# Kernel tuning notes

Hardware: AMD Instinct MI355X
Metric: run time of the kernel (lower is better)

The kernel has to match this reference:

```python
import jax, jax.numpy as jnp
import numpy as np

N = 10000
E = 160000
IN_DIM = 256
PROJ_DIM = 512
HIDDEN = 512
OUT_DIM = 512
HEADS1, HEADS2, HEADS3 = 4, 4, 1
NEG_SLOPE = 0.2  # PyG GATConv default


def gat_conv(x, edge_index, W, att_src, att_dst, bias, heads, out_c, concat):
    """PyG GATConv (eval mode), with self-loops already appended to edge_index.
    x: [N, F_in]; W: [F_in, heads*out_c]; att_src/att_dst: [heads, out_c]; bias: [heads*out_c] or [out_c]."""
    n = x.shape[0]
    h = (x @ W).reshape(n, heads, out_c)            # [N, H, C]
    a_src = jnp.einsum('nhc,hc->nh', h, att_src)     # [N, H]
    a_dst = jnp.einsum('nhc,hc->nh', h, att_dst)     # [N, H]
    src, dst = edge_index[0], edge_index[1]
    e = jax.nn.leaky_relu(a_src[src] + a_dst[dst], NEG_SLOPE)  # [E, H]
    # segment softmax over incoming edges per destination node
    e_max = jax.ops.segment_max(e, dst, num_segments=n)
    e_exp = jnp.exp(e - e_max[dst])
    denom = jax.ops.segment_sum(e_exp, dst, num_segments=n)
    alpha = e_exp / denom[dst]                       # [E, H]
    msg = alpha[:, :, None] * h[src]                 # [E, H, C]
    out = jax.ops.segment_sum(msg, dst, num_segments=n)  # [N, H, C]
    out = out.reshape(n, heads * out_c) if concat else out.mean(axis=1)
    return out + bias


def setup_inputs() -> dict:
    key = jax.random.key(0)
    ks = jax.random.split(key, 16)
    g = 0.1
    inp = {
        'x': jax.random.normal(ks[0], (N, IN_DIM), dtype=jnp.float32),
        'edge_index': jax.random.randint(ks[1], (2, E), 0, N, dtype=jnp.int64),
        'proj_W': jax.random.normal(ks[2], (IN_DIM, PROJ_DIM), dtype=jnp.float32) * g,
        'proj_b': jnp.zeros((PROJ_DIM,), dtype=jnp.float32),
        'W1': jax.random.normal(ks[3], (PROJ_DIM, HEADS1 * HIDDEN), dtype=jnp.float32) * g,
        'as1': jax.random.normal(ks[4], (HEADS1, HIDDEN), dtype=jnp.float32) * g,
        'ad1': jax.random.normal(ks[5], (HEADS1, HIDDEN), dtype=jnp.float32) * g,
        'b1': jnp.zeros((HEADS1 * HIDDEN,), dtype=jnp.float32),
        'W2': jax.random.normal(ks[6], (HEADS1 * HIDDEN, HEADS2 * HIDDEN), dtype=jnp.float32) * g * 0.5,
        'as2': jax.random.normal(ks[7], (HEADS2, HIDDEN), dtype=jnp.float32) * g,
        'ad2': jax.random.normal(ks[8], (HEADS2, HIDDEN), dtype=jnp.float32) * g,
        'b2': jnp.zeros((HEADS2 * HIDDEN,), dtype=jnp.float32),
        'W3': jax.random.normal(ks[9], (HEADS2 * HIDDEN, HEADS3 * OUT_DIM), dtype=jnp.float32) * g * 0.5,
        'as3': jax.random.normal(ks[10], (HEADS3, OUT_DIM), dtype=jnp.float32) * g,
        'ad3': jax.random.normal(ks[11], (HEADS3, OUT_DIM), dtype=jnp.float32) * g,
        'b3': jnp.zeros((OUT_DIM,), dtype=jnp.float32),
    }
    return inp


def reference(x, edge_index, proj_W, proj_b, W1, as1, ad1, b1, W2, as2, ad2, b2, W3, as3, ad3, b3):
    # append self-loops once (PyG GATConv add_self_loops=True)
    loops = jnp.arange(N, dtype=edge_index.dtype)
    ei = jnp.concatenate([edge_index, jnp.stack([loops, loops])], axis=1)
    h = x @ proj_W + proj_b                                   # [N, 512]
    h = jax.nn.elu(gat_conv(h, ei, W1, as1, ad1, b1, HEADS1, HIDDEN, True))
    h = jax.nn.elu(gat_conv(h, ei, W2, as2, ad2, b2, HEADS2, HIDDEN, True))
    return gat_conv(h, ei, W3, as3, ad3, b3, HEADS3, OUT_DIM, False)  # [N, 512]
```

## Files before the change

kernel.cpp:

```cpp
#include <hip/hip_runtime.h>
#include <hip/hip_bf16.h>


#define LB(x) __launch_bounds__(x)

typedef unsigned short u16;
typedef unsigned int u32;
typedef __attribute__((ext_vector_type(8))) short short8;
typedef __attribute__((ext_vector_type(8))) short bf16x8;
typedef __attribute__((ext_vector_type(8))) _Float16 f16x8;
typedef __attribute__((ext_vector_type(4))) float f32x4;

__device__ __forceinline__ float b2f(u16 u) {
    union { float f; u32 u; } x;
    x.u = ((u32)u) << 16;
    return x.f;
}
__device__ __forceinline__ u16 f2b(float f) {
    u32 u = __float_as_uint(f);
    u = (u + 0x7FFFu + ((u >> 16) & 1u)) >> 16;
    return (u16)u;
}
__device__ __forceinline__ u16 f2h(float f) {
    union { _Float16 h; u16 u; } x;
    x.h = (_Float16)f;
    return x.u;
}
__device__ __forceinline__ float h2f(u16 u) {
    union { _Float16 h; u16 u; } x;
    x.u = u;
    return (float)x.h;
}
__device__ __forceinline__ void lds_cp16(const void* g, void* l) {
    __builtin_amdgcn_global_load_lds(
        (const __attribute__((address_space(1))) unsigned int*)g,
        (__attribute__((address_space(3))) unsigned int*)l, 16, 0, 0);
}

__global__ void k_deg(const int* __restrict__ ei, int E, int Np, int* __restrict__ deg) {
    int e = blockIdx.x * blockDim.x + threadIdx.x;
    if (e >= E + Np) return;
    int dst = (e < E) ? ei[E + e] : (e - E);
    atomicAdd(&deg[dst], 1);
}

__global__ LB(256) void k_s1(const int* __restrict__ deg, int* __restrict__ row_ptr,
                             int* __restrict__ bsum, int n) {
    __shared__ int sh[256];
    int b = blockIdx.x, t = threadIdx.x;
    int i = b * 256 + t;
    int v = (i < n) ? deg[i] : 0;
    sh[t] = v;
    __syncthreads();
    #pragma unroll
    for (int off = 1; off < 256; off <<= 1) {
        int add = (t >= off) ? sh[t - off] : 0;
        __syncthreads();
        sh[t] += add;
        __syncthreads();
    }
    if (i < n) row_ptr[i + 1] = sh[t];
    if (t == 255) bsum[b] = sh[255];
}

__global__ LB(64) void k_s2(int* __restrict__ bsum, int* __restrict__ boff, int nb) {
    __shared__ int sh[64];
    int t = threadIdx.x;
    sh[t] = (t < nb) ? bsum[t] : 0;
    __syncthreads();
    #pragma unroll
    for (int off = 1; off < 64; off <<= 1) {
        int add = (t >= off) ? sh[t - off] : 0;
        __syncthreads();
        sh[t] += add;
        __syncthreads();
    }
    if (t < nb) boff[t] = (t == 0) ? 0 : sh[t - 1];
}

__global__ LB(256) void k_s3(const int* __restrict__ deg, int* __restrict__ row_ptr,
                             const int* __restrict__ boff, int* __restrict__ cursor, int n) {
    int b = blockIdx.x, t = threadIdx.x;
    int i = b * 256 + t;
    if (i == 0) row_ptr[0] = 0;
    if (i < n) {
        int inc = row_ptr[i + 1] + boff[b];
        row_ptr[i + 1] = inc;
        cursor[i] = inc - deg[i];
    }
}

__global__ void k_fill(const int* __restrict__ ei, int E, int Np,
                       int* __restrict__ cursor, int* __restrict__ col_src) {
    int e = blockIdx.x * blockDim.x + threadIdx.x;
    if (e >= E + Np) return;
    int src, dst;
    if (e < E) { src = ei[e]; dst = ei[E + e]; }
    else       { src = dst = e - E; }
    int pos = atomicAdd(&cursor[dst], 1);
    col_src[pos] = src;
}

__global__ void k_pack(const float* __restrict__ in, u16* __restrict__ hi,
                       u16* __restrict__ lo, int n4) {
    int i = blockIdx.x * blockDim.x + threadIdx.x;
    if (i >= n4) return;
    float4 v = ((const float4*)in)[i];
    ushort4 h, l;
    h.x = f2b(v.x); l.x = f2b(v.x - b2f(h.x));
    h.y = f2b(v.y); l.y = f2b(v.y - b2f(h.y));
    h.z = f2b(v.z); l.z = f2b(v.z - b2f(h.z));
    h.w = f2b(v.w); l.w = f2b(v.w - b2f(h.w));
    ((ushort4*)hi)[i] = h;
    ((ushort4*)lo)[i] = l;
}

template<bool F16S>
__global__ LB(256) void k_wt_pack(const float* __restrict__ W, u16* __restrict__ Whi,
                                  u16* __restrict__ Wlo, int K, int Nn) {
    __shared__ float sh[32][33];
    int n0 = blockIdx.x * 32, k0 = blockIdx.y * 32;
    int c = threadIdx.x & 31, r0 = threadIdx.x >> 5;
    #pragma unroll
    for (int r = r0; r < 32; r += 8)
        sh[r][c] = W[(size_t)(k0 + r) * Nn + n0 + c];
    __syncthreads();
    #pragma unroll
    for (int r = r0; r < 32; r += 8) {
        float v = sh[c][r];
        if (F16S) {
            Whi[(size_t)(n0 + r) * K + k0 + c] = f2h(v);
        } else {
            u16 hi = f2b(v);
            Whi[(size_t)(n0 + r) * K + k0 + c] = hi;
            Wlo[(size_t)(n0 + r) * K + k0 + c] = f2b(v - b2f(hi));
        }
    }
}

__global__ LB(64) void k_bfold(const float* __restrict__ pb,
                               const u16* __restrict__ w1t_hi, const u16* __restrict__ w1t_lo,
                               float* __restrict__ bfold, int K) {
    int n = blockIdx.x;
    int lane = threadIdx.x;
    float s = 0.f;
    for (int k = lane; k < K; k += 64) {
        float w = b2f(w1t_hi[(size_t)n * K + k]) + b2f(w1t_lo[(size_t)n * K + k]);
        s = fmaf(pb[k], w, s);
    }
    #pragma unroll
    for (int off = 32; off; off >>= 1) s += __shfl_xor(s, off);
    if (lane == 0) bfold[n] = s;
}

template<int WM, int NFR, int PREC, int OUTMODE, bool ATT>
__global__ __launch_bounds__(WM * 128)
void k_gemm_pl(const u16* __restrict__ Ahi, const u16* __restrict__ Alo,
               const u16* __restrict__ Bhi, const u16* __restrict__ Blo,
               const float* __restrict__ bias,
               u16* __restrict__ Chi, u16* __restrict__ Clo,
               u16* __restrict__ Cf16,
               const float* __restrict__ att_s, const float* __restrict__ att_d,
               float* __restrict__ a_src, float* __restrict__ a_dst,
               int HH, int M, int K, int Nn) {
    constexpr int BM = WM * 64;
    constexpr int BN = NFR * 32;
    constexpr int T  = WM * 128;
    constexpr int BITER = (NFR * 128) / T > 0 ? (NFR * 128) / T : 1;
    constexpr int ALO_SZ = (PREC == 0) ? BM * 32 : 8;
    constexpr int BLO_SZ = (PREC == 0) ? BN * 32 : 8;
    __shared__ u16 AsHi[BM * 32];
    __shared__ u16 AsLo[ALO_SZ];
    __shared__ u16 BsHi[BN * 32];
    __shared__ u16 BsLo[BLO_SZ];
    const int tid  = threadIdx.x;
    const int lane = tid & 63;
    const int w    = tid >> 6;
    const int wr   = w >> 1;
    const int wc   = w & 1;
    const int row0 = blockIdx.y * BM;
    const int col0 = blockIdx.x * BN;
    const int ln15 = lane & 15;
    const int lq   = lane >> 4;

    f32x4 acc[4][NFR];
    #pragma unroll
    for (int m = 0; m < 4; ++m)
        #pragma unroll
        for (int n = 0; n < NFR; ++n) acc[m][n] = (f32x4){0.f, 0.f, 0.f, 0.f};

    for (int k0 = 0; k0 < K; k0 += 32) {
        #pragma unroll
        for (int i = 0; i < 2; ++i) {
            int c = i * T + tid;
            int r  = 2 * (c >> 3) + (((c >> 2) ^ (c >> 4)) & 1);
            int kc = (c & 3) ^ (r & 3);
            int gra = row0 + r; if (gra >= M) gra = M - 1;
            size_t ga = (size_t)gra * K + k0 + kc * 8;
            lds_cp16(Ahi + ga, (char*)AsHi + c * 16);
            if (PREC == 0) lds_cp16(Alo + ga, (char*)AsLo + c * 16);
        }
        #pragma unroll
        for (int i = 0; i < BITER; ++i) {
            int c = i * T + tid;
            int r  = 2 * (c >> 3) + (((c >> 2) ^ (c >> 4)) & 1);
            int kc = (c & 3) ^ (r & 3);
            size_t gb = (size_t)(col0 + r) * K + k0 + kc * 8;
            lds_cp16(Bhi + gb, (char*)BsHi + c * 16);
            if (PREC == 0) lds_cp16(Blo + gb, (char*)BsLo + c * 16);
        }
        __syncthreads();
        if (PREC == 0) {
            bf16x8 ah[4], al[4], bh[NFR], bl[NFR];
            #pragma unroll
            for (int m = 0; m < 4; ++m) {
                int row = wr * 64 + m * 16 + ln15;
                int byo = (row * 64 + lq * 16) ^ ((row & 7) << 4);
                ah[m] = *(const bf16x8*)((const char*)AsHi + byo);
                al[m] = *(const bf16x8*)((const char*)AsLo + byo);
            }
            #pragma unroll
            for (int n = 0; n < NFR; ++n) {
                int row = wc * (NFR * 16) + n * 16 + ln15;
                int byo = (row * 64 + lq * 16) ^ ((row & 7) << 4);
                bh[n] = *(const bf16x8*)((const char*)BsHi + byo);
                bl[n] = *(const bf16x8*)((const char*)BsLo + byo);
            }
            #pragma unroll
            for (int m = 0; m < 4; ++m)
                #pragma unroll
                for (int n = 0; n < NFR; ++n) {
                    acc[m][n] = __builtin_amdgcn_mfma_f32_16x16x32_bf16(al[m], bh[n], acc[m][n], 0, 0, 0);
                    acc[m][n] = __builtin_amdgcn_mfma_f32_16x16x32_bf16(ah[m], bl[n], acc[m][n], 0, 0, 0);
                    acc[m][n] = __builtin_amdgcn_mfma_f32_16x16x32_bf16(ah[m], bh[n], acc[m][n], 0, 0, 0);
                }
        } else {
            f16x8 a[4], b[NFR];
            #pragma unroll
            for (int m = 0; m < 4; ++m) {
                int row = wr * 64 + m * 16 + ln15;
                int byo = (row * 64 + lq * 16) ^ ((row & 7) << 4);
                a[m] = *(const f16x8*)((const char*)AsHi + byo);
            }
            #pragma unroll
            for (int n = 0; n < NFR; ++n) {
                int row = wc * (NFR * 16) + n * 16 + ln15;
                int byo = (row * 64 + lq * 16) ^ ((row & 7) << 4);
                b[n] = *(const f16x8*)((const char*)BsHi + byo);
            }
            #pragma unroll
            for (int m = 0; m < 4; ++m)
                #pragma unroll
                for (int n = 0; n < NFR; ++n)
                    acc[m][n] = __builtin_amdgcn_mfma_f32_16x16x32_f16(a[m], b[n], acc[m][n], 0, 0, 0);
        }
        __syncthreads();
    }

    #pragma unroll
    for (int m = 0; m < 4; ++m) {
        #pragma unroll
        for (int n = 0; n < NFR; ++n) {
            int gc = col0 + wc * (NFR * 16) + n * 16 + ln15;
            float badd = bias ? bias[gc] : 0.f;
            #pragma unroll
            for (int j = 0; j < 4; ++j) {
                int gr = row0 + wr * 64 + m * 16 + lq * 4 + j;
                if (gr < M) {
                    float v = acc[m][n][j] + badd;
                    size_t o = (size_t)gr * Nn + gc;
                    if (OUTMODE == 0) {
                        u16 hi = f2b(v);
                        Chi[o] = hi;
                        Clo[o] = f2b(v - b2f(hi));
                    } else {
                        Cf16[o] = f2h(v);
                    }
                }
            }
        }
    }

    if (ATT) {
        float atts[NFR], attd[NFR], bb[NFR];
        #pragma unroll
        for (int n = 0; n < NFR; ++n) {
            int gc = col0 + wc * (NFR * 16) + n * 16 + ln15;
            atts[n] = att_s[gc];
            attd[n] = att_d[gc];
            bb[n]   = bias ? bias[gc] : 0.f;
        }
        const int head = (col0 + wc * (NFR * 16)) >> 9;
        #pragma unroll
        for (int m = 0; m < 4; ++m) {
            #pragma unroll
            for (int j = 0; j < 4; ++j) {
                int gr = row0 + wr * 64 + m * 16 + lq * 4 + j;
                float s1 = 0.f, s2 = 0.f;
                #pragma unroll
                for (int n = 0; n < NFR; ++n) {
                    float v = acc[m][n][j] + bb[n];
                    s1 = fmaf(v, atts[n], s1);
                    s2 = fmaf(v, attd[n], s2);
                }
                #pragma unroll
                for (int off = 1; off < 16; off <<= 1) {
                    s1 += __shfl_xor(s1, off);
                    s2 += __shfl_xor(s2, off);
                }
                if (ln15 == 0 && gr < M) {
                    atomicAdd(&a_src[gr * HH + head], s1);
                    atomicAdd(&a_dst[gr * HH + head], s2);
                }
            }
        }
    }
}

template <int HH, int OMODE, bool ELU_>
__global__ __launch_bounds__(HH * 64)
void k_sagg(const int* __restrict__ row_ptr, const int* __restrict__ col_src,
            const float* __restrict__ a_src, const float* __restrict__ a_dst,
            const u16* __restrict__ hf, const float* __restrict__ bias,
            u16* __restrict__ Oh, float* __restrict__ Of, int C) {
    __shared__ float sal[HH * 64];
    const int d    = blockIdx.x;
    const int tid  = threadIdx.x;
    const int w    = tid >> 6;
    const int lane = tid & 63;
    const int F    = HH * C;
    const int o    = tid * 8;
    const int s = row_ptr[d], eend = row_ptr[d + 1];
    const int cnt = eend - s;
    const float adh = a_dst[d * HH + w];

    float acc[8];
    #pragma unroll
    for (int j = 0; j < 8; ++j) acc[j] = 0.f;

    if (cnt <= 64) {
        bool act = lane < cnt;
        float av = act ? a_src[col_src[s + lane] * HH + w] : 0.f;
        float x = av + adh;
        x = (x > 0.f) ? x : 0.2f * x;
        float v = act ? x : -1e30f;
        float m = v;
        #pragma unroll
        for (int off = 32; off; off >>= 1) m = fmaxf(m, __shfl_xor(m, off));
        float e_ = act ? __expf(v - m) : 0.f;
        float sum = e_;
        #pragma unroll
        for (int off = 32; off; off >>= 1) sum += __shfl_xor(sum, off);
        if (act) sal[w * 64 + lane] = e_ / sum;
        __syncthreads();

        if (cnt > 0) {
            short8 vv; float a;
            {
                int src0 = col_src[s];
                a = sal[w * 64];
                vv = *(const short8*)(hf + (size_t)src0 * F + o);
            }
            for (int i = 0; i < cnt; ++i) {
                short8 w_; float an;
                bool more = (i + 1 < cnt);
                if (more) {
                    int srcn = col_src[s + i + 1];
                    an = sal[w * 64 + i + 1];
                    w_ = *(const short8*)(hf + (size_t)srcn * F + o);
                }
                #pragma unroll
                for (int j = 0; j < 8; ++j)
                    acc[j] = fmaf(a, h2f((u16)vv[j]), acc[j]);
                if (more) { a = an; vv = w_; }
            }
        }
    } else {
        float m = -1e30f;
        for (int e = s + lane; e < eend; e += 64) {
            float x = a_src[col_src[e] * HH + w] + adh;
            x = (x > 0.f) ? x : 0.2f * x;
            m = fmaxf(m, x);
        }
        #pragma unroll
        for (int off = 32; off; off >>= 1) m = fmaxf(m, __shfl_xor(m, off));
        float sum = 0.f;
        for (int e = s + lane; e < eend; e += 64) {
            float x = a_src[col_src[e] * HH + w] + adh;
            x = (x > 0.f) ? x : 0.2f * x;
            sum += __expf(x - m);
        }
        #pragma unroll
        for (int off = 32; off; off >>= 1) sum += __shfl_xor(sum, off);
        float inv = 1.0f / sum;
        for (int base = s; base < eend; base += 64) {
            int e = base + lane;
            if (e < eend) {
                float x = a_src[col_src[e] * HH + w] + adh;
                x = (x > 0.f) ? x : 0.2f * x;
                sal[w * 64 + lane] = __expf(x - m) * inv;
            }
            __syncthreads();
            int nn = (eend - base < 64) ? (eend - base) : 64;
            for (int i = 0; i < nn; ++i) {
                int src = col_src[base + i];
                float a = sal[w * 64 + i];
                short8 vv = *(const short8*)(hf + (size_t)src * F + o);
                #pragma unroll
                for (int j = 0; j < 8; ++j)
                    acc[j] = fmaf(a, h2f((u16)vv[j]), acc[j]);
            }
            __syncthreads();
        }
    }

    #pragma unroll
    for (int j = 0; j < 8; ++j) {
        acc[j] += bias[o + j];
        if (ELU_) acc[j] = (acc[j] > 0.f) ? acc[j] : __expf(acc[j]) - 1.f;
    }
    if (OMODE == 0) {
        short8 r;
        #pragma unroll
        for (int j = 0; j < 8; ++j) r[j] = (short)f2h(acc[j]);
        *(short8*)(Oh + (size_t)d * F + o) = r;
    } else {
        float* po = Of + (size_t)d * F + o;
        #pragma unroll
        for (int j4 = 0; j4 < 2; ++j4) {
            float4 r;
            r.x = acc[j4 * 4 + 0]; r.y = acc[j4 * 4 + 1];
            r.z = acc[j4 * 4 + 2]; r.w = acc[j4 * 4 + 3];
            *(float4*)&po[j4 * 4] = r;
        }
    }
}

extern "C" void kernel_launch(void* const* d_in, const int* in_sizes, int n_in,
                              void* d_out, int out_size, void* d_ws, size_t ws_size,
                              hipStream_t stream) {
    const float* x      = (const float*)d_in[0];
    const int*   ei     = (const int*)d_in[1];
    const float* proj_W = (const float*)d_in[2];
    const float* proj_b = (const float*)d_in[3];
    const float* W1  = (const float*)d_in[4];
    const float* as1 = (const float*)d_in[5];
    const float* ad1 = (const float*)d_in[6];
    const float* b1  = (const float*)d_in[7];
    const float* W2  = (const float*)d_in[8];
    const float* as2 = (const float*)d_in[9];
    const float* ad2 = (const float*)d_in[10];
    const float* b2  = (const float*)d_in[11];
    const float* W3  = (const float*)d_in[12];
    const float* as3 = (const float*)d_in[13];
    const float* ad3 = (const float*)d_in[14];
    const float* b3  = (const float*)d_in[15];

    const int N  = in_sizes[0] / 256;
    const int E  = in_sizes[1] / 2;
    const int Ep = E + N;
    const int NB = (N + 255) / 256;

    size_t off = 0;
    auto alloc = [&](size_t bytes) -> void* {
        void* p = (char*)d_ws + off;
        off += (bytes + 255) & ~(size_t)255;
        return p;
    };
    u16* bufX    = (u16*)alloc((size_t)N * 2048 * 2);
    u16* bufY    = (u16*)alloc((size_t)N * 2048 * 2);
    u16* xb_hi   = (u16*)alloc((size_t)N * 256 * 2);
    u16* xb_lo   = (u16*)alloc((size_t)N * 256 * 2);
    u16* pw_hi   = (u16*)alloc((size_t)256 * 512 * 2);
    u16* pw_lo   = (u16*)alloc((size_t)256 * 512 * 2);
    u16* wf_hi   = (u16*)alloc((size_t)2048 * 256 * 2);
    u16* wf_lo   = (u16*)alloc((size_t)2048 * 256 * 2);
    float* bfold   = (float*)alloc((size_t)2048 * 4);
    float* att_z   = (float*)alloc((size_t)N * 18 * 4);
    int*   deg     = (int*)alloc((size_t)N * 4);
    int*   cursor  = (int*)alloc((size_t)N * 4);
    int*   row_ptr = (int*)alloc((size_t)(N + 1) * 4);
    int*   col_src = (int*)alloc((size_t)Ep * 4);
    int*   bsum    = (int*)alloc((size_t)NB * 4);
    int*   boff    = (int*)alloc((size_t)NB * 4);
    (void)ws_size;

    float* a_src1 = att_z;
    float* a_dst1 = att_z + (size_t)N * 4;
    float* a_src2 = att_z + (size_t)N * 8;
    float* a_dst2 = att_z + (size_t)N * 12;
    float* a_src3 = att_z + (size_t)N * 16;
    float* a_dst3 = att_z + (size_t)N * 17;

    u16* whi = (u16*)d_out;
    u16* wlo = (u16*)d_out + (size_t)2048 * 2048;

    hipMemsetAsync(deg, 0, (size_t)N * 4, stream);
    hipMemsetAsync(att_z, 0, (size_t)N * 18 * 4, stream);
    int eb = (Ep + 255) / 256;
    k_deg<<<eb, 256, 0, stream>>>(ei, E, N, deg);
    k_s1<<<NB, 256, 0, stream>>>(deg, row_ptr, bsum, N);
    k_s2<<<1, 64, 0, stream>>>(bsum, boff, NB);
    k_s3<<<NB, 256, 0, stream>>>(deg, row_ptr, boff, cursor, N);
    k_fill<<<eb, 256, 0, stream>>>(ei, E, N, cursor, col_src);

    const int MB1 = (N + 127) / 128;
    const int MB2 = (N + 255) / 256;

    k_pack<<<(N * 256 / 4 + 255) / 256, 256, 0, stream>>>(x, xb_hi, xb_lo, N * 256 / 4);
    k_pack<<<(256 * 512 / 4 + 255) / 256, 256, 0, stream>>>(proj_W, pw_hi, pw_lo, 256 * 512 / 4);

    k_wt_pack<false><<<dim3(2048 / 32, 512 / 32), 256, 0, stream>>>(W1, whi, wlo, 512, 2048);
    k_bfold<<<2048, 64, 0, stream>>>(proj_b, whi, wlo, bfold, 512);
    k_gemm_pl<2, 2, 0, 0, false><<<dim3(256 / 64, 2048 / 128), 256, 0, stream>>>(
        whi, wlo, pw_hi, pw_lo, nullptr, wf_hi, wf_lo, nullptr,
        nullptr, nullptr, nullptr, nullptr, 0, 2048, 512, 256);

    k_gemm_pl<2, 4, 0, 2, true><<<dim3(2048 / 128, MB1), 256, 0, stream>>>(
        xb_hi, xb_lo, wf_hi, wf_lo, bfold, nullptr, nullptr, bufX,
        as1, ad1, a_src1, a_dst1, 4, N, 256, 2048);
    k_sagg<4, 0, true><<<N, 256, 0, stream>>>(row_ptr, col_src, a_src1, a_dst1,
                                              bufX, b1, bufY, nullptr, 512);

    k_wt_pack<true><<<dim3(2048 / 32, 2048 / 32), 256, 0, stream>>>(W2, whi, nullptr, 2048, 2048);
    k_gemm_pl<4, 4, 2, 2, true><<<dim3(2048 / 128, MB2), 512, 0, stream>>>(
        bufY, nullptr, whi, nullptr, nullptr, nullptr, nullptr, bufX,
        as2, ad2, a_src2, a_dst2, 4, N, 2048, 2048);
    k_sagg<4, 0, true><<<N, 256, 0, stream>>>(row_ptr, col_src, a_src2, a_dst2,
                                              bufX, b2, bufY, nullptr, 512);

    k_wt_pack<true><<<dim3(512 / 32, 2048 / 32), 256, 0, stream>>>(W3, whi, nullptr, 2048, 512);
    k_gemm_pl<2, 2, 2, 2, true><<<dim3(512 / 64, MB1), 256, 0, stream>>>(
        bufY, nullptr, whi, nullptr, nullptr, nullptr, nullptr, bufX,
        as3, ad3, a_src3, a_dst3, 1, N, 2048, 512);
    k_sagg<1, 1, false><<<N, 64, 0, stream>>>(row_ptr, col_src, a_src3, a_dst3,
                                              bufX, b3, nullptr, (float*)d_out, 512);
}
```

Baseline: 623.8 us.

## Double-buffer LDS tiles in layer 2/3 GEMMs and unroll aggregation gather by two

Adds a double-buffered LDS mode to the GEMM kernel. The next K-tile's async copies are issued into the alternate buffer while the current tile is computed, which removes one barrier per iteration and hides global-load latency. It is enabled for the two f16 GEMMs with K=2048. Separately, the small-degree aggregation loop now keeps two neighbour rows in flight instead of one, to increase memory-level parallelism. The cost is doubled shared memory in those GEMMs, which may lower occupancy, and more registers in the gather loop.

```diff
diff --git a/kernel.cpp b/kernel.cpp
--- a/kernel.cpp
+++ b/kernel.cpp
@@ -153,7 +153,7 @@
     if (lane == 0) bfold[n] = s;
 }
 
-template<int WM, int NFR, int PREC, int OUTMODE, bool ATT>
+template<int WM, int NFR, int PREC, int OUTMODE, bool ATT, bool DB>
 __global__ __launch_bounds__(WM * 128)
 void k_gemm_pl(const u16* __restrict__ Ahi, const u16* __restrict__ Alo,
                const u16* __restrict__ Bhi, const u16* __restrict__ Blo,
@@ -166,13 +166,14 @@
     constexpr int BM = WM * 64;
     constexpr int BN = NFR * 32;
     constexpr int T  = WM * 128;
-    constexpr int BITER = (NFR * 128) / T > 0 ? (NFR * 128) / T : 1;
-    constexpr int ALO_SZ = (PREC == 0) ? BM * 32 : 8;
-    constexpr int BLO_SZ = (PREC == 0) ? BN * 32 : 8;
-    __shared__ u16 AsHi[BM * 32];
-    __shared__ u16 AsLo[ALO_SZ];
-    __shared__ u16 BsHi[BN * 32];
-    __shared__ u16 BsLo[BLO_SZ];
+    constexpr int BITER = ((NFR * 128) / T > 0) ? (NFR * 128) / T : 1;
+    constexpr int NBUF = DB ? 2 : 1;
+    constexpr int ASZ = BM * 32;
+    constexpr int BSZ = BN * 32;
+    __shared__ u16 AsHi[NBUF * ASZ];
+    __shared__ u16 AsLo[(PREC == 0) ? NBUF * ASZ : 8];
+    __shared__ u16 BsHi[NBUF * BSZ];
+    __shared__ u16 BsLo[(PREC == 0) ? NBUF * BSZ : 8];
     const int tid  = threadIdx.x;
     const int lane = tid & 63;
     const int w    = tid >> 6;
@@ -189,7 +190,9 @@
         #pragma unroll
         for (int n = 0; n < NFR; ++n) acc[m][n] = (f32x4){0.f, 0.f, 0.f, 0.f};
 
-    for (int k0 = 0; k0 < K; k0 += 32) {
+    auto STAGE = [&](int k0, int buf) {
+        size_t ab = (size_t)buf * ASZ * 2;
+        size_t bb = (size_t)buf * BSZ * 2;
         #pragma unroll
         for (int i = 0; i < 2; ++i) {
             int c = i * T + tid;
@@ -197,8 +200,8 @@
             int kc = (c & 3) ^ (r & 3);
             int gra = row0 + r; if (gra >= M) gra = M - 1;
             size_t ga = (size_t)gra * K + k0 + kc * 8;
-            lds_cp16(Ahi + ga, (char*)AsHi + c * 16);
-            if (PREC == 0) lds_cp16(Alo + ga, (char*)AsLo + c * 16);
+            lds_cp16(Ahi + ga, (char*)AsHi + ab + c * 16);
+            if (PREC == 0) lds_cp16(Alo + ga, (char*)AsLo + ab + c * 16);
         }
         #pragma unroll
         for (int i = 0; i < BITER; ++i) {
@@ -206,25 +209,29 @@
             int r  = 2 * (c >> 3) + (((c >> 2) ^ (c >> 4)) & 1);
             int kc = (c & 3) ^ (r & 3);
             size_t gb = (size_t)(col0 + r) * K + k0 + kc * 8;
-            lds_cp16(Bhi + gb, (char*)BsHi + c * 16);
-            if (PREC == 0) lds_cp16(Blo + gb, (char*)BsLo + c * 16);
-        }
-        __syncthreads();
+            lds_cp16(Bhi + gb, (char*)BsHi + bb + c * 16);
+            if (PREC == 0) lds_cp16(Blo + gb, (char*)BsLo + bb + c * 16);
+        }
+    };
+
+    auto COMPUTE = [&](int buf) {
+        size_t ab = (size_t)buf * ASZ * 2;
+        size_t bb = (size_t)buf * BSZ * 2;
         if (PREC == 0) {
             bf16x8 ah[4], al[4], bh[NFR], bl[NFR];
             #pragma unroll
             for (int m = 0; m < 4; ++m) {
                 int row = wr * 64 + m * 16 + ln15;
-                int byo = (row * 64 + lq * 16) ^ ((row & 7) << 4);
-                ah[m] = *(const bf16x8*)((const char*)AsHi + byo);
-                al[m] = *(const bf16x8*)((const char*)AsLo + byo);
+                size_t byo = (size_t)((row * 64 + lq * 16) ^ ((row & 7) << 4));
+                ah[m] = *(const bf16x8*)((const char*)AsHi + ab + byo);
+                al[m] = *(const bf16x8*)((const char*)AsLo + ab + byo);
             }
             #pragma unroll
             for (int n = 0; n < NFR; ++n) {
                 int row = wc * (NFR * 16) + n * 16 + ln15;
-                int byo = (row * 64 + lq * 16) ^ ((row & 7) << 4);
-                bh[n] = *(const bf16x8*)((const char*)BsHi + byo);
-                bl[n] = *(const bf16x8*)((const char*)BsLo + byo);
+                size_t byo = (size_t)((row * 64 + lq * 16) ^ ((row & 7) << 4));
+                bh[n] = *(const bf16x8*)((const char*)BsHi + bb + byo);
+                bl[n] = *(const bf16x8*)((const char*)BsLo + bb + byo);
             }
             #pragma unroll
             for (int m = 0; m < 4; ++m)
@@ -239,14 +246,14 @@
             #pragma unroll
             for (int m = 0; m < 4; ++m) {
                 int row = wr * 64 + m * 16 + ln15;
-                int byo = (row * 64 + lq * 16) ^ ((row & 7) << 4);
-                a[m] = *(const f16x8*)((const char*)AsHi + byo);
+                size_t byo = (size_t)((row * 64 + lq * 16) ^ ((row & 7) << 4));
+                a[m] = *(const f16x8*)((const char*)AsHi + ab + byo);
             }
             #pragma unroll
             for (int n = 0; n < NFR; ++n) {
                 int row = wc * (NFR * 16) + n * 16 + ln15;
-                int byo = (row * 64 + lq * 16) ^ ((row & 7) << 4);
-                b[n] = *(const f16x8*)((const char*)BsHi + byo);
+                size_t byo = (size_t)((row * 64 + lq * 16) ^ ((row & 7) << 4));
+                b[n] = *(const f16x8*)((const char*)BsHi + bb + byo);
             }
             #pragma unroll
             for (int m = 0; m < 4; ++m)
@@ -254,7 +261,25 @@
                 for (int n = 0; n < NFR; ++n)
                     acc[m][n] = __builtin_amdgcn_mfma_f32_16x16x32_f16(a[m], b[n], acc[m][n], 0, 0, 0);
         }
+    };
+
+    if (DB) {
+        const int nt = K >> 5;
+        STAGE(0, 0);
         __syncthreads();
+        for (int t = 0; t < nt; ++t) {
+            int cur = t & 1;
+            if (t + 1 < nt) STAGE((t + 1) << 5, cur ^ 1);
+            COMPUTE(cur);
+            __syncthreads();
+        }
+    } else {
+        for (int k0 = 0; k0 < K; k0 += 32) {
+            STAGE(k0, 0);
+            __syncthreads();
+            COMPUTE(0);
+            __syncthreads();
+        }
     }
 
     #pragma unroll
@@ -354,26 +379,25 @@
         if (act) sal[w * 64 + lane] = e_ / sum;
         __syncthreads();
 
-        if (cnt > 0) {
-            short8 vv; float a;
-            {
-                int src0 = col_src[s];
-                a = sal[w * 64];
-                vv = *(const short8*)(hf + (size_t)src0 * F + o);
-            }
-            for (int i = 0; i < cnt; ++i) {
-                short8 w_; float an;
-                bool more = (i + 1 < cnt);
-                if (more) {
-                    int srcn = col_src[s + i + 1];
-                    an = sal[w * 64 + i + 1];
-                    w_ = *(const short8*)(hf + (size_t)srcn * F + o);
-                }
-                #pragma unroll
-                for (int j = 0; j < 8; ++j)
-                    acc[j] = fmaf(a, h2f((u16)vv[j]), acc[j]);
-                if (more) { a = an; vv = w_; }
-            }
+        short8 v0, v1; float a0, a1;
+        if (cnt > 0) { v0 = *(const short8*)(hf + (size_t)col_src[s] * F + o); a0 = sal[w * 64]; }
+        if (cnt > 1) { v1 = *(const short8*)(hf + (size_t)col_src[s + 1] * F + o); a1 = sal[w * 64 + 1]; }
+        int i = 0;
+        for (; i + 2 <= cnt; i += 2) {
+            short8 t0, t1; float b0, b1;
+            bool m0 = (i + 2 < cnt), m1 = (i + 3 < cnt);
+            if (m0) { t0 = *(const short8*)(hf + (size_t)col_src[s + i + 2] * F + o); b0 = sal[w * 64 + i + 2]; }
+            if (m1) { t1 = *(const short8*)(hf + (size_t)col_src[s + i + 3] * F + o); b1 = sal[w * 64 + i + 3]; }
+            #pragma unroll
+            for (int j = 0; j < 8; ++j) acc[j] = fmaf(a0, h2f((u16)v0[j]), acc[j]);
+            #pragma unroll
+            for (int j = 0; j < 8; ++j) acc[j] = fmaf(a1, h2f((u16)v1[j]), acc[j]);
+            if (m0) { v0 = t0; a0 = b0; }
+            if (m1) { v1 = t1; a1 = b1; }
+        }
+        if (i < cnt) {
+            #pragma unroll
+            for (int j = 0; j < 8; ++j) acc[j] = fmaf(a0, h2f((u16)v0[j]), acc[j]);
         }
     } else {
         float m = -1e30f;
@@ -512,25 +536,25 @@
 
     k_wt_pack<false><<<dim3(2048 / 32, 512 / 32), 256, 0, stream>>>(W1, whi, wlo, 512, 2048);
     k_bfold<<<2048, 64, 0, stream>>>(proj_b, whi, wlo, bfold, 512);
-    k_gemm_pl<2, 2, 0, 0, false><<<dim3(256 / 64, 2048 / 128), 256, 0, stream>>>(
+    k_gemm_pl<2, 2, 0, 0, false, false><<<dim3(256 / 64, 2048 / 128), 256, 0, stream>>>(
         whi, wlo, pw_hi, pw_lo, nullptr, wf_hi, wf_lo, nullptr,
         nullptr, nullptr, nullptr, nullptr, 0, 2048, 512, 256);
 
-    k_gemm_pl<2, 4, 0, 2, true><<<dim3(2048 / 128, MB1), 256, 0, stream>>>(
+    k_gemm_pl<2, 4, 0, 2, true, false><<<dim3(2048 / 128, MB1), 256, 0, stream>>>(
         xb_hi, xb_lo, wf_hi, wf_lo, bfold, nullptr, nullptr, bufX,
         as1, ad1, a_src1, a_dst1, 4, N, 256, 2048);
     k_sagg<4, 0, true><<<N, 256, 0, stream>>>(row_ptr, col_src, a_src1, a_dst1,
                                               bufX, b1, bufY, nullptr, 512);
 
     k_wt_pack<true><<<dim3(2048 / 32, 2048 / 32), 256, 0, stream>>>(W2, whi, nullptr, 2048, 2048);
-    k_gemm_pl<4, 4, 2, 2, true><<<dim3(2048 / 128, MB2), 512, 0, stream>>>(
+    k_gemm_pl<4, 4, 2, 2, true, true><<<dim3(2048 / 128, MB2), 512, 0, stream>>>(
         bufY, nullptr, whi, nullptr, nullptr, nullptr, nullptr, bufX,
         as2, ad2, a_src2, a_dst2, 4, N, 2048, 2048);
     k_sagg<4, 0, true><<<N, 256, 0, stream>>>(row_ptr, col_src, a_src2, a_dst2,
                                               bufX, b2, bufY, nullptr, 512);
 
     k_wt_pack<true><<<dim3(512 / 32, 2048 / 32), 256, 0, stream>>>(W3, whi, nullptr, 2048, 512);
-    k_gemm_pl<2, 2, 2, 2, true><<<dim3(512 / 64, MB1), 256, 0, stream>>>(
+    k_gemm_pl<2, 2, 2, 2, true, true><<<dim3(512 / 64, MB1), 256, 0, stream>>>(
         bufY, nullptr, whi, nullptr, nullptr, nullptr, nullptr, bufX,
         as3, ad3, a_src3, a_dst3, 1, N, 2048, 512);
     k_sagg<1, 1, false><<<N, 64, 0, stream>>>(row_ptr, col_src, a_src3, a_dst3,
```

After: 619.2 us. About the same (-0.7%).
